# Kernel tuning notes

Hardware: AMD Instinct MI355X
Metric: run time of the kernel (lower is better)

## Reference

```python
import jax, jax.numpy as jnp
import numpy as np

N = 50000      # nodes
E = 800000     # edges (avg degree 16)
D_IN = 96
D_OUT = 96


def setup_inputs() -> dict:
    key = jax.random.key(0)
    k1, k2, k3, k4 = jax.random.split(key, 4)
    x = jax.random.normal(k1, (N, D_IN), dtype=jnp.float32)
    edge_index = jax.random.randint(k2, (2, E), 0, N, dtype=jnp.int32)
    scale = 1.0 / np.sqrt(D_IN)
    Wl = jax.random.normal(k3, (D_OUT, D_IN), dtype=jnp.float32) * scale  # lin_l weight (neighbors)
    bl = jnp.zeros((D_OUT,), dtype=jnp.float32)                           # lin_l bias
    Wr = jax.random.normal(k4, (D_OUT, D_IN), dtype=jnp.float32) * scale  # lin_r weight (root), no bias
    return {"x": x, "edge_index": edge_index, "Wl": Wl, "bl": bl, "Wr": Wr}


def reference(x, edge_index, Wl, bl, Wr):
    # SAGEConv (mean aggr): z = lin_l(mean_{j in N(i)} x_j) + lin_r(x_i), then ReLU.
    # Dropout p=0.0 -> identity.
    src, dst = edge_index[0], edge_index[1]  # messages flow src -> dst (PyG convention)
    msg = x[src]  # [E, D_IN] gather
    agg = jax.ops.segment_sum(msg, dst, num_segments=N)                     # [N, D_IN]
    deg = jax.ops.segment_sum(jnp.ones((E, 1), x.dtype), dst, num_segments=N)  # [N, 1]
    agg = agg / jnp.maximum(deg, 1.0)  # mean; isolated nodes -> 0
    z = agg @ Wl.T + bl + x @ Wr.T     # [N, D_OUT]
    return jax.nn.relu(z)
```

## Files before the change

kernel.cpp:

```cpp
#include <hip/hip_runtime.h>
#include <hip/hip_bf16.h>

#define D 96
#define CAP 32
#define NB1 256
#define BUKSHIFT 5
#define BUKN 32
#define CAPB 1024
#define NBUK_MAX 2048
#define KMAX 7
#define OVL_MAX 256

typedef __attribute__((ext_vector_type(8))) short bf16x8;
typedef __attribute__((ext_vector_type(4))) float f32x4;
typedef unsigned u32x3 __attribute__((ext_vector_type(3), aligned(4)));

__device__ __forceinline__ short f2bf(float f)
{
    union { __hip_bfloat16 h; short s; } u;
    u.h = __float2bfloat16(f);
    return u.s;
}

__device__ __forceinline__ bf16x8 load_frag(const float* p)
{
    float4 lo = *(const float4*)p;
    float4 hi = *(const float4*)(p + 4);
    bf16x8 r;
    r[0] = f2bf(lo.x); r[1] = f2bf(lo.y); r[2] = f2bf(lo.z); r[3] = f2bf(lo.w);
    r[4] = f2bf(hi.x); r[5] = f2bf(hi.y); r[6] = f2bf(hi.z); r[7] = f2bf(hi.w);
    return r;
}

__device__ __forceinline__ float bf_lo(unsigned p) { return __uint_as_float(p << 16); }
__device__ __forceinline__ float bf_hi(unsigned p) { return __uint_as_float(p & 0xFFFF0000u); }

__global__ __launch_bounds__(256) void init_kernel(
    const float* __restrict__ Wl, const float* __restrict__ Wr,
    __hip_bfloat16* __restrict__ wbf, int* __restrict__ bcnt, int nbuk)
{
    const int idx = blockIdx.x * 256 + threadIdx.x;
    if (idx < nbuk) bcnt[idx] = 0;
    if (idx < 2304) {
        int mat = idx / 1152;
        int rem = idx - mat * 1152;
        int n  = rem / 12;
        int k8 = rem - n * 12;
        const float* Wp = mat ? Wr : Wl;
        bf16x8 v = load_frag(Wp + (size_t)n * D + k8 * 8);
        int ct = n >> 4, m = n & 15, kt = k8 >> 2, quad = k8 & 3;
        ((bf16x8*)wbf)[(mat * 18 + ct * 3 + kt) * 64 + quad * 16 + m] = v;
    }
}

__global__ __launch_bounds__(256) void p2_gemm(
    const int* __restrict__ src, const int* __restrict__ dst,
    int* __restrict__ bcnt, unsigned* __restrict__ ebuf,
    const float* __restrict__ x, const __hip_bfloat16* __restrict__ wbf,
    __hip_bfloat16* __restrict__ hl, float* __restrict__ hr,
    int nbuk, int N, int E)
{
    if (blockIdx.x < NB1) {
        __shared__ int mo[NBUK_MAX];
        const int t = threadIdx.x;
        for (int i = t; i < nbuk; i += 256) mo[i] = 0;
        __syncthreads();
        const int CS = (E + NB1 - 1) / NB1;
        const int base = blockIdx.x * CS;
        int lim = E - base; if (lim > CS) lim = CS; if (lim < 0) lim = 0;
        for (int i = t; i < lim; i += 256)
            atomicAdd(&mo[dst[base + i] >> BUKSHIFT], 1);
        __syncthreads();
        int c7[KMAX], b7[KMAX];
        #pragma unroll
        for (int k = 0; k < KMAX; ++k) {
            int i = t + k * 256;
            c7[k] = (i < nbuk) ? mo[i] : 0;
        }
        #pragma unroll
        for (int k = 0; k < KMAX; ++k) {
            int i = t + k * 256;
            b7[k] = (i < nbuk) ? atomicAdd(&bcnt[i], c7[k]) : 0;
        }
        #pragma unroll
        for (int k = 0; k < KMAX; ++k) {
            int i = t + k * 256;
            if (i < nbuk) mo[i] = i * CAPB + b7[k];
        }
        __syncthreads();
        for (int i = t; i < lim; i += 256) {
            int e = base + i;
            int d = dst[e], s = src[e];
            int bu = d >> BUKSHIFT;
            int g = atomicAdd(&mo[bu], 1);
            if (g < (bu + 1) * CAPB)
                ebuf[g] = (unsigned)s | ((unsigned)(d & (BUKN - 1)) << 16);
        }
        return;
    }

    const int gk = blockIdx.x - NB1;
    const int gwave = (gk * 256 + threadIdx.x) >> 6;
    const int nrt = N / 16;
    if (gwave >= nrt) return;
    const int lane = threadIdx.x & 63;
    const int m = lane & 15, quad = lane >> 4;
    const int row = gwave * 16 + m;
    const bf16x8* wb = (const bf16x8*)wbf;

    bf16x8 a[3];
    #pragma unroll
    for (int kt = 0; kt < 3; ++kt)
        a[kt] = load_frag(x + (size_t)row * D + kt * 32 + quad * 8);

    const int orow = gwave * 16 + quad * 4;
    #pragma unroll
    for (int ct = 0; ct < 6; ++ct) {
        f32x4 accl = {0.f, 0.f, 0.f, 0.f};
        f32x4 accr = {0.f, 0.f, 0.f, 0.f};
        #pragma unroll
        for (int kt = 0; kt < 3; ++kt)
            accl = __builtin_amdgcn_mfma_f32_16x16x32_bf16(
                a[kt], wb[(ct * 3 + kt) * 64 + lane], accl, 0, 0, 0);
        #pragma unroll
        for (int kt = 0; kt < 3; ++kt)
            accr = __builtin_amdgcn_mfma_f32_16x16x32_bf16(
                a[kt], wb[(18 + ct * 3 + kt) * 64 + lane], accr, 0, 0, 0);
        int col = ct * 16 + m;
        int sl = col / 24, c = col - sl * 24;
        #pragma unroll
        for (int r = 0; r < 4; ++r) {
            int node = orow + r;
            hl[((size_t)sl * N + node) * 32 + c] = __float2bfloat16(accl[r]);
            hr[(size_t)node * D + col] = accr[r];
        }
    }
}

__global__ __launch_bounds__(256) void p3agg(
    const unsigned* __restrict__ ebuf, const int* __restrict__ bcnt,
    const __hip_bfloat16* __restrict__ hl, const float* __restrict__ bl,
    float* __restrict__ out, int nbuk, int N)
{
    const int xcd = blockIdx.x & 7;
    const int s  = xcd >> 1;
    const int bu = ((blockIdx.x >> 3) << 1) | (xcd & 1);
    if (bu >= nbuk) return;

    __shared__ int cl[BUKN];
    __shared__ unsigned short sl[BUKN * CAP];
    __shared__ unsigned ovl[OVL_MAX];
    __shared__ int ovc;
    const int t = threadIdx.x;
    if (t < BUKN) cl[t] = 0;
    if (t == 0) ovc = 0;
    __syncthreads();

    const int n = min(bcnt[bu], CAPB);
    const unsigned* eb = ebuf + (size_t)bu * CAPB;
    for (int i = t; i < n; i += 256) {
        unsigned e = eb[i];
        int dl = e >> 16, sv = (int)(e & 0xFFFFu);
        int pos = atomicAdd(&cl[dl], 1);
        if (pos < CAP) {
            sl[dl * CAP + pos] = (unsigned short)sv;
        } else {
            int o = atomicAdd(&ovc, 1);
            if (o < OVL_MAX) ovl[o] = e;
        }
    }
    __syncthreads();

    const int wv = t >> 6, lane = t & 63;
    const int nn = lane >> 4;
    const int e4 = (lane >> 2) & 3;
    const int r  = lane & 3;
    const unsigned short* hs = (const unsigned short*)hl + (size_t)s * N * 32;
    const int o = s * 24 + r * 6;
    const float b0 = bl[o],     b1 = bl[o + 1], b2 = bl[o + 2];
    const float b3 = bl[o + 3], b4 = bl[o + 4], b5 = bl[o + 5];
    const int novc = min(ovc, OVL_MAX);

    for (int q = wv * 2; q < wv * 2 + 2; ++q) {
        const int nq = q * 4;
        const int deg = cl[nq + nn];
        const int dcm = min(deg, CAP);
        int um = max(max(cl[nq], cl[nq + 1]), max(cl[nq + 2], cl[nq + 3]));
        um = min(um, CAP);

        float a0 = 0.f, a1 = 0.f, a2 = 0.f, a3 = 0.f, a4 = 0.f, a5 = 0.f;
        #pragma unroll 2
        for (int j = 0; j < um; j += 4) {
            int idx = j + e4;
            bool act = idx < dcm;
            int nb = act ? (int)sl[(nq + nn) * CAP + idx] : 0;
            u32x3 p = *(const u32x3*)((const char*)hs + (size_t)nb * 64 + r * 12);
            float mk = act ? 1.f : 0.f;
            a0 += mk * bf_lo(p.x); a1 += mk * bf_hi(p.x);
            a2 += mk * bf_lo(p.y); a3 += mk * bf_hi(p.y);
            a4 += mk * bf_lo(p.z); a5 += mk * bf_hi(p.z);
        }
        #pragma unroll
        for (int off = 4; off <= 8; off <<= 1) {
            a0 += __shfl_xor(a0, off); a1 += __shfl_xor(a1, off);
            a2 += __shfl_xor(a2, off); a3 += __shfl_xor(a3, off);
            a4 += __shfl_xor(a4, off); a5 += __shfl_xor(a5, off);
        }
        if (e4 == 0) {
            const int node = (bu << BUKSHIFT) + nq + nn;
            if (node < N) {
                for (int k = 0; k < novc; ++k) {
                    unsigned e = ovl[k];
                    if ((int)(e >> 16) == nq + nn) {
                        int nb = (int)(e & 0xFFFFu);
                        u32x3 p = *(const u32x3*)((const char*)hs + (size_t)nb * 64 + r * 12);
                        a0 += bf_lo(p.x); a1 += bf_hi(p.x);
                        a2 += bf_lo(p.y); a3 += bf_hi(p.y);
                        a4 += bf_lo(p.z); a5 += bf_hi(p.z);
                    }
                }
                const float inv = 1.0f / fmaxf((float)deg, 1.0f);
                float* op = out + (size_t)node * D + o;
                float2 u0 = *(const float2*)op;
                float2 u1 = *(const float2*)(op + 2);
                float2 u2 = *(const float2*)(op + 4);
                u0.x = fmaxf(a0 * inv + b0 + u0.x, 0.f);
                u0.y = fmaxf(a1 * inv + b1 + u0.y, 0.f);
                u1.x = fmaxf(a2 * inv + b2 + u1.x, 0.f);
                u1.y = fmaxf(a3 * inv + b3 + u1.y, 0.f);
                u2.x = fmaxf(a4 * inv + b4 + u2.x, 0.f);
                u2.y = fmaxf(a5 * inv + b5 + u2.y, 0.f);
                *(float2*)op       = u0;
                *(float2*)(op + 2) = u1;
                *(float2*)(op + 4) = u2;
            }
        }
    }
}

extern "C" void kernel_launch(void* const* d_in, const int* in_sizes, int n_in,
                              void* d_out, int out_size, void* d_ws, size_t ws_size,
                              hipStream_t stream)
{
    const float* x  = (const float*)d_in[0];
    const int*   ei = (const int*)d_in[1];
    const float* Wl = (const float*)d_in[2];
    const float* bl = (const float*)d_in[3];
    const float* Wr = (const float*)d_in[4];
    float* out = (float*)d_out;

    const int N = in_sizes[0] / D;
    const int E = in_sizes[1] / 2;
    const int* src = ei;
    const int* dst = ei + E;
    const int nbuk = (N + BUKN - 1) >> BUKSHIFT;

    char* p = (char*)d_ws;
    __hip_bfloat16* wbf = (__hip_bfloat16*)p;    p += 36864;
    __hip_bfloat16* hl  = (__hip_bfloat16*)p;    p += (size_t)4 * N * 32 * 2;
    int* bcnt = (int*)p;                         p += ((size_t)nbuk * 4 + 255) / 256 * 256;
    unsigned* ebuf = (unsigned*)p;

    init_kernel<<<9, 256, 0, stream>>>(Wl, Wr, wbf, bcnt, nbuk);

    const int nrt = N / 16;
    const int gemmb = (nrt + 3) / 4;
    p2_gemm<<<NB1 + gemmb, 256, 0, stream>>>(
        src, dst, bcnt, ebuf, x, wbf, hl, out, nbuk, N, E);

    const int aggb = ((nbuk + 1) / 2) * 8;
    p3agg<<<aggb, 256, 0, stream>>>(ebuf, bcnt, hl, bl, out, nbuk, N);
}
```

Before: 133.7 us.

## Slice root projection per XCD and interleave two node groups in aggregation

The root-term GEMM output now goes to a separate workspace buffer laid out in the same per-XCD column slices as the neighbor projection, so each aggregation block reads a compact, slice-local region instead of a strided read of the output array. The aggregation loop also processes both of a wave's 4-node groups in one loop, with two sets of accumulators, to put more independent gathers in flight per iteration. This costs an extra 19 MB workspace buffer and more registers, and the loop now runs to the max degree over eight nodes rather than four.

```diff
diff --git a/kernel.cpp b/kernel.cpp
--- a/kernel.cpp
+++ b/kernel.cpp
@@ -57,7 +57,7 @@
     const int* __restrict__ src, const int* __restrict__ dst,
     int* __restrict__ bcnt, unsigned* __restrict__ ebuf,
     const float* __restrict__ x, const __hip_bfloat16* __restrict__ wbf,
-    __hip_bfloat16* __restrict__ hl, float* __restrict__ hr,
+    __hip_bfloat16* __restrict__ hl, float* __restrict__ hrs,
     int nbuk, int N, int E)
 {
     if (blockIdx.x < NB1) {
@@ -132,15 +132,15 @@
         for (int r = 0; r < 4; ++r) {
             int node = orow + r;
             hl[((size_t)sl * N + node) * 32 + c] = __float2bfloat16(accl[r]);
-            hr[(size_t)node * D + col] = accr[r];
+            hrs[((size_t)sl * N + node) * 24 + c] = accr[r];
         }
     }
 }
 
 __global__ __launch_bounds__(256) void p3agg(
     const unsigned* __restrict__ ebuf, const int* __restrict__ bcnt,
-    const __hip_bfloat16* __restrict__ hl, const float* __restrict__ bl,
-    float* __restrict__ out, int nbuk, int N)
+    const __hip_bfloat16* __restrict__ hl, const float* __restrict__ hrs,
+    const float* __restrict__ bl, float* __restrict__ out, int nbuk, int N)
 {
     const int xcd = blockIdx.x & 7;
     const int s  = xcd >> 1;
@@ -176,37 +176,54 @@
     const int e4 = (lane >> 2) & 3;
     const int r  = lane & 3;
     const unsigned short* hs = (const unsigned short*)hl + (size_t)s * N * 32;
+    const float* hp = hrs + (size_t)s * N * 24;
     const int o = s * 24 + r * 6;
     const float b0 = bl[o],     b1 = bl[o + 1], b2 = bl[o + 2];
     const float b3 = bl[o + 3], b4 = bl[o + 4], b5 = bl[o + 5];
     const int novc = min(ovc, OVL_MAX);
 
-    for (int q = wv * 2; q < wv * 2 + 2; ++q) {
-        const int nq = q * 4;
-        const int deg = cl[nq + nn];
-        const int dcm = min(deg, CAP);
-        int um = max(max(cl[nq], cl[nq + 1]), max(cl[nq + 2], cl[nq + 3]));
-        um = min(um, CAP);
-
-        float a0 = 0.f, a1 = 0.f, a2 = 0.f, a3 = 0.f, a4 = 0.f, a5 = 0.f;
-        #pragma unroll 2
-        for (int j = 0; j < um; j += 4) {
-            int idx = j + e4;
-            bool act = idx < dcm;
-            int nb = act ? (int)sl[(nq + nn) * CAP + idx] : 0;
-            u32x3 p = *(const u32x3*)((const char*)hs + (size_t)nb * 64 + r * 12);
-            float mk = act ? 1.f : 0.f;
-            a0 += mk * bf_lo(p.x); a1 += mk * bf_hi(p.x);
-            a2 += mk * bf_lo(p.y); a3 += mk * bf_hi(p.y);
-            a4 += mk * bf_lo(p.z); a5 += mk * bf_hi(p.z);
-        }
-        #pragma unroll
-        for (int off = 4; off <= 8; off <<= 1) {
-            a0 += __shfl_xor(a0, off); a1 += __shfl_xor(a1, off);
-            a2 += __shfl_xor(a2, off); a3 += __shfl_xor(a3, off);
-            a4 += __shfl_xor(a4, off); a5 += __shfl_xor(a5, off);
-        }
-        if (e4 == 0) {
+    const int nqA = wv * 8;
+    const int nqB = wv * 8 + 4;
+    const int degA = cl[nqA + nn], degB = cl[nqB + nn];
+    const int dcmA = min(degA, CAP), dcmB = min(degB, CAP);
+    int umA = max(max(cl[nqA], cl[nqA + 1]), max(cl[nqA + 2], cl[nqA + 3]));
+    int umB = max(max(cl[nqB], cl[nqB + 1]), max(cl[nqB + 2], cl[nqB + 3]));
+    int um = min(max(umA, umB), CAP);
+
+    float a0 = 0.f, a1 = 0.f, a2 = 0.f, a3 = 0.f, a4 = 0.f, a5 = 0.f;
+    float c0 = 0.f, c1 = 0.f, c2 = 0.f, c3 = 0.f, c4 = 0.f, c5 = 0.f;
+    #pragma unroll 2
+    for (int j = 0; j < um; j += 4) {
+        int idx = j + e4;
+        bool actA = idx < dcmA, actB = idx < dcmB;
+        int nbA = actA ? (int)sl[(nqA + nn) * CAP + idx] : 0;
+        int nbB = actB ? (int)sl[(nqB + nn) * CAP + idx] : 0;
+        u32x3 pA = *(const u32x3*)((const char*)hs + (size_t)nbA * 64 + r * 12);
+        u32x3 pB = *(const u32x3*)((const char*)hs + (size_t)nbB * 64 + r * 12);
+        float mA = actA ? 1.f : 0.f, mB = actB ? 1.f : 0.f;
+        a0 += mA * bf_lo(pA.x); a1 += mA * bf_hi(pA.x);
+        a2 += mA * bf_lo(pA.y); a3 += mA * bf_hi(pA.y);
+        a4 += mA * bf_lo(pA.z); a5 += mA * bf_hi(pA.z);
+        c0 += mB * bf_lo(pB.x); c1 += mB * bf_hi(pB.x);
+        c2 += mB * bf_lo(pB.y); c3 += mB * bf_hi(pB.y);
+        c4 += mB * bf_lo(pB.z); c5 += mB * bf_hi(pB.z);
+    }
+    #pragma unroll
+    for (int off = 4; off <= 8; off <<= 1) {
+        a0 += __shfl_xor(a0, off); c0 += __shfl_xor(c0, off);
+        a1 += __shfl_xor(a1, off); c1 += __shfl_xor(c1, off);
+        a2 += __shfl_xor(a2, off); c2 += __shfl_xor(c2, off);
+        a3 += __shfl_xor(a3, off); c3 += __shfl_xor(c3, off);
+        a4 += __shfl_xor(a4, off); c4 += __shfl_xor(c4, off);
+        a5 += __shfl_xor(a5, off); c5 += __shfl_xor(c5, off);
+    }
+    if (e4 == 0) {
+        #pragma unroll
+        for (int half = 0; half < 2; ++half) {
+            const int nq = half ? nqB : nqA;
+            const int deg = half ? degB : degA;
+            float v0 = half ? c0 : a0, v1 = half ? c1 : a1, v2 = half ? c2 : a2;
+            float v3 = half ? c3 : a3, v4 = half ? c4 : a4, v5 = half ? c5 : a5;
             const int node = (bu << BUKSHIFT) + nq + nn;
             if (node < N) {
                 for (int k = 0; k < novc; ++k) {
@@ -214,22 +231,24 @@
                     if ((int)(e >> 16) == nq + nn) {
                         int nb = (int)(e & 0xFFFFu);
                         u32x3 p = *(const u32x3*)((const char*)hs + (size_t)nb * 64 + r * 12);
-                        a0 += bf_lo(p.x); a1 += bf_hi(p.x);
-                        a2 += bf_lo(p.y); a3 += bf_hi(p.y);
-                        a4 += bf_lo(p.z); a5 += bf_hi(p.z);
+                        v0 += bf_lo(p.x); v1 += bf_hi(p.x);
+                        v2 += bf_lo(p.y); v3 += bf_hi(p.y);
+                        v4 += bf_lo(p.z); v5 += bf_hi(p.z);
                     }
                 }
                 const float inv = 1.0f / fmaxf((float)deg, 1.0f);
+                const float* rp = hp + (size_t)node * 24 + r * 6;
+                float2 h0 = *(const float2*)rp;
+                float2 h1 = *(const float2*)(rp + 2);
+                float2 h2 = *(const float2*)(rp + 4);
                 float* op = out + (size_t)node * D + o;
-                float2 u0 = *(const float2*)op;
-                float2 u1 = *(const float2*)(op + 2);
-                float2 u2 = *(const float2*)(op + 4);
-                u0.x = fmaxf(a0 * inv + b0 + u0.x, 0.f);
-                u0.y = fmaxf(a1 * inv + b1 + u0.y, 0.f);
-                u1.x = fmaxf(a2 * inv + b2 + u1.x, 0.f);
-                u1.y = fmaxf(a3 * inv + b3 + u1.y, 0.f);
-                u2.x = fmaxf(a4 * inv + b4 + u2.x, 0.f);
-                u2.y = fmaxf(a5 * inv + b5 + u2.y, 0.f);
+                float2 u0, u1, u2;
+                u0.x = fmaxf(v0 * inv + b0 + h0.x, 0.f);
+                u0.y = fmaxf(v1 * inv + b1 + h0.y, 0.f);
+                u1.x = fmaxf(v2 * inv + b2 + h1.x, 0.f);
+                u1.y = fmaxf(v3 * inv + b3 + h1.y, 0.f);
+                u2.x = fmaxf(v4 * inv + b4 + h2.x, 0.f);
+                u2.y = fmaxf(v5 * inv + b5 + h2.y, 0.f);
                 *(float2*)op       = u0;
                 *(float2*)(op + 2) = u1;
                 *(float2*)(op + 4) = u2;
@@ -258,6 +277,7 @@
     char* p = (char*)d_ws;
     __hip_bfloat16* wbf = (__hip_bfloat16*)p;    p += 36864;
     __hip_bfloat16* hl  = (__hip_bfloat16*)p;    p += (size_t)4 * N * 32 * 2;
+    float* hrs = (float*)p;                      p += (size_t)4 * N * 24 * 4;
     int* bcnt = (int*)p;                         p += ((size_t)nbuk * 4 + 255) / 256 * 256;
     unsigned* ebuf = (unsigned*)p;
 
@@ -266,8 +286,8 @@
     const int nrt = N / 16;
     const int gemmb = (nrt + 3) / 4;
     p2_gemm<<<NB1 + gemmb, 256, 0, stream>>>(
-        src, dst, bcnt, ebuf, x, wbf, hl, out, nbuk, N, E);
+        src, dst, bcnt, ebuf, x, wbf, hl, hrs, nbuk, N, E);
 
     const int aggb = ((nbuk + 1) / 2) * 8;
-    p3agg<<<aggb, 256, 0, stream>>>(ebuf, bcnt, hl, bl, out, nbuk, N);
-}
+    p3agg<<<aggb, 256, 0, stream>>>(ebuf, bcnt, hl, hrs, bl, out, nbuk, N);
+}
```

After: 132.5 us. No clear change (-0.9%).
